# Optimization experiments

Hardware: AMD Instinct MI355X
Metric: run time of the kernel (lower is better)

## Reference

```python
import jax, jax.numpy as jnp
import numpy as np

WIN = 7          # window_size
DIM = 192        # embedding dim
HEADS = 6
HEAD_DIM = DIM // HEADS
B_ = 4096        # batch * num_windows
N = WIN * WIN    # tokens per window


def _relative_position_index():
    coords = np.stack(np.meshgrid(np.arange(WIN), np.arange(WIN), indexing='ij'))  # [2,7,7]
    flat = coords.reshape(2, -1)                                                   # [2,49]
    rel = flat[:, :, None] - flat[:, None, :]                                      # [2,49,49]
    rel = rel.transpose(1, 2, 0).astype(np.int32)                                  # [49,49,2]
    rel[:, :, 0] += WIN - 1
    rel[:, :, 1] += WIN - 1
    rel[:, :, 0] *= 2 * WIN - 1
    return jnp.asarray(rel.sum(-1), dtype=jnp.int32)                               # [49,49]


def setup_inputs() -> dict:
    key = jax.random.key(0)
    ks = jax.random.split(key, 6)
    std = 0.02
    return {
        'x': jax.random.normal(ks[0], (B_, N, DIM), dtype=jnp.float32),
        'qkv_w': jax.random.normal(ks[1], (3 * DIM, DIM), dtype=jnp.float32) * std,
        'qkv_b': jnp.zeros((3 * DIM,), dtype=jnp.float32),
        'proj_w': jax.random.normal(ks[2], (DIM, DIM), dtype=jnp.float32) * std,
        'proj_b': jnp.zeros((DIM,), dtype=jnp.float32),
        'bias_table': jax.random.normal(ks[3], ((2 * WIN - 1) ** 2, HEADS), dtype=jnp.float32) * std,
        'rel_index': _relative_position_index(),
    }


def reference(x, qkv_w, qkv_b, proj_w, proj_b, bias_table, rel_index):
    B, n, C = x.shape
    # qkv projection -> [3, B, H, N, hd]
    qkv = (x @ qkv_w.T + qkv_b).reshape(B, n, 3, HEADS, HEAD_DIM)
    qkv = jnp.transpose(qkv, (2, 0, 3, 1, 4))
    q, k, v = qkv[0], qkv[1], qkv[2]
    # relative position bias: [H, N, N]
    bias = bias_table[rel_index.reshape(-1)].reshape(n, n, HEADS)
    bias = jnp.transpose(bias, (2, 0, 1))[None]  # [1, H, N, N]
    scale = 1.0 / jnp.sqrt(jnp.asarray(HEAD_DIM, dtype=x.dtype))
    logits = jnp.einsum('bhnd,bhmd->bhnm', q, k) * scale + bias
    attn = jax.nn.softmax(logits, axis=-1)
    out = jnp.einsum('bhnm,bhmd->bhnd', attn, v)
    out = jnp.transpose(out, (0, 2, 1, 3)).reshape(B, n, C)
    return out @ proj_w.T + proj_b
```

## Files before the change

### kernel.cpp

```cpp
#include <hip/hip_runtime.h>

#define NTOK 49
#define DIM 192
#define HEADS 6
#define HD 32

typedef __bf16 bf16x8 __attribute__((ext_vector_type(8)));
typedef float f32x4 __attribute__((ext_vector_type(4)));

#define WPROJ_USH 110592
#define BIAS_BYTE 294912

#define SCALE 0.17677669529663687f

__device__ __forceinline__ unsigned short f2bf(float f) {
    unsigned int u = __builtin_bit_cast(unsigned int, f);
    u += 0x7fffu + ((u >> 16) & 1u);
    return (unsigned short)(u >> 16);
}
__device__ __forceinline__ unsigned int pack2(float a, float b) {
    return (unsigned int)f2bf(a) | ((unsigned int)f2bf(b) << 16);
}

__global__ void prep(const float* __restrict__ qkv_w, const float* __restrict__ proj_w,
                     const float* __restrict__ bias_table, const int* __restrict__ rel_index,
                     unsigned short* __restrict__ w16, float* __restrict__ bias_cd) {
    int bid = blockIdx.x;
    if (bid < 72) {
        int c = bid * 256 + threadIdx.x;
        const float* src; unsigned short* dst; int OT; int cc; int isq = 0;
        if (c < 13824)      { src = qkv_w;  dst = w16;             OT = 36; cc = c; isq = 1; }
        else                { src = proj_w; dst = w16 + WPROJ_USH; OT = 12; cc = c - 13824; }
        int lane = cc & 63;
        int t = cc >> 6;
        int ot = t % OT, ks = t / OT;
        int f  = ot * 16 + (lane & 15);
        int k0 = ks * 32 + (lane >> 4) * 8;
        float sc = (isq && f < 192) ? SCALE : 1.0f;
        const float* p = src + (size_t)f * DIM + k0;
        float4 a = *(const float4*)p;
        float4 b = *(const float4*)(p + 4);
        uint4 o;
        o.x = pack2(a.x * sc, a.y * sc); o.y = pack2(a.z * sc, a.w * sc);
        o.z = pack2(b.x * sc, b.y * sc); o.w = pack2(b.z * sc, b.w * sc);
        *(uint4*)(dst + (size_t)cc * 8) = o;
    } else {
        int gid = (bid - 72) * 256 + threadIdx.x;
        int lane = gid & 63;
        int tile = (gid >> 6) & 15;
        int h    = gid >> 10;
        int kt = tile >> 2, qt = tile & 3;
        int qtok = qt * 16 + (lane & 15);
        int key0 = kt * 16 + (lane >> 4) * 4;
        float4 v;
        float* vp = (float*)&v;
        for (int r = 0; r < 4; ++r) {
            int key = key0 + r;
            float val;
            if (key >= NTOK)       val = -1e30f;
            else if (qtok >= NTOK) val = 0.0f;
            else                   val = bias_table[rel_index[qtok * NTOK + key] * HEADS + h];
            vp[r] = val;
        }
        *(float4*)(bias_cd + (size_t)gid * 4) = v;
    }
}

#define SCR_OFF 24576
#define LDS_BYTES 49152

__global__ __launch_bounds__(384, 3) void win_attn(
    const float* __restrict__ x,
    const float* __restrict__ qkv_b,
    const float* __restrict__ proj_b,
    const unsigned short* __restrict__ wq16,
    const unsigned short* __restrict__ wp16,
    const float* __restrict__ bias_cd,
    float* __restrict__ out)
{
    extern __shared__ char smem[];
    const int tid  = threadIdx.x;
    const int lane = tid & 63;
    const int h    = tid >> 6;
    const int l15  = lane & 15;
    const int quad = lane >> 4;
    const int b    = blockIdx.x;

    for (int i = 0; i < 4; ++i) {
        int c  = tid + i * 384;
        int cl = c & 63;
        int mt = (c >> 6) & 3;
        int ks = c >> 8;
        int tok = mt * 16 + (cl & 15);
        int d0  = ks * 32 + (cl >> 4) * 8;
        uint4 o = {0u, 0u, 0u, 0u};
        if (tok < NTOK) {
            const float* p = x + ((size_t)b * NTOK + tok) * DIM + d0;
            float4 a  = *(const float4*)p;
            float4 bb = *(const float4*)(p + 4);
            o.x = pack2(a.x, a.y); o.y = pack2(a.z, a.w);
            o.z = pack2(bb.x, bb.y); o.w = pack2(bb.z, bb.w);
        }
        *(uint4*)(smem + (size_t)c * 16) = o;
    }
    __syncthreads();

    char* buf = smem + SCR_OFF + h * 4096;

    f32x4 qa[2][4], ka[2][4];
    for (int ft = 0; ft < 2; ++ft)
        for (int nt = 0; nt < 4; ++nt) { qa[ft][nt] = (f32x4){0,0,0,0}; ka[ft][nt] = (f32x4){0,0,0,0}; }
    for (int ks = 0; ks < 6; ++ks) {
        int4 xf[4];
        for (int nt = 0; nt < 4; ++nt)
            xf[nt] = *(const int4*)(smem + (((ks*4 + nt)*64 + lane) << 4));
        int4 wq[2], wk[2];
        for (int ft = 0; ft < 2; ++ft) {
            wq[ft] = *(const int4*)(wq16 + ((size_t)((ks*36      + h*2 + ft)*64 + lane) << 3));
            wk[ft] = *(const int4*)(wq16 + ((size_t)((ks*36 + 12 + h*2 + ft)*64 + lane) << 3));
        }
        for (int ft = 0; ft < 2; ++ft)
            for (int nt = 0; nt < 4; ++nt) {
                qa[ft][nt] = __builtin_amdgcn_mfma_f32_16x16x32_bf16(
                    __builtin_bit_cast(bf16x8, wq[ft]), __builtin_bit_cast(bf16x8, xf[nt]), qa[ft][nt], 0, 0, 0);
                ka[ft][nt] = __builtin_amdgcn_mfma_f32_16x16x32_bf16(
                    __builtin_bit_cast(bf16x8, wk[ft]), __builtin_bit_cast(bf16x8, xf[nt]), ka[ft][nt], 0, 0, 0);
            }
    }

    int4 qf[4], kf[4];
    for (int ft = 0; ft < 2; ++ft) {
        float4 bias = *(const float4*)(qkv_b + (h*2 + ft)*16 + quad*4);
        int quadp = ft*2 + (quad >> 1);
        for (int nt = 0; nt < 4; ++nt) {
            uint2 w;
            w.x = pack2(qa[ft][nt][0] + bias.x*SCALE, qa[ft][nt][1] + bias.y*SCALE);
            w.y = pack2(qa[ft][nt][2] + bias.z*SCALE, qa[ft][nt][3] + bias.w*SCALE);
            *(uint2*)(buf + nt*1024 + (l15 + 16*quadp)*16 + (quad & 1)*8) = w;
        }
    }
    for (int qt = 0; qt < 4; ++qt)
        qf[qt] = *(const int4*)(buf + qt*1024 + lane*16);
    for (int ft = 0; ft < 2; ++ft) {
        float4 bias = *(const float4*)(qkv_b + 192 + (h*2 + ft)*16 + quad*4);
        int quadp = ft*2 + (quad >> 1);
        for (int nt = 0; nt < 4; ++nt) {
            uint2 w;
            w.x = pack2(ka[ft][nt][0] + bias.x, ka[ft][nt][1] + bias.y);
            w.y = pack2(ka[ft][nt][2] + bias.z, ka[ft][nt][3] + bias.w);
            *(uint2*)(buf + nt*1024 + (l15 + 16*quadp)*16 + (quad & 1)*8) = w;
        }
    }
    for (int kt = 0; kt < 4; ++kt)
        kf[kt] = *(const int4*)(buf + kt*1024 + lane*16);

    f32x4 s[4][4];
    for (int kt = 0; kt < 4; ++kt)
        for (int qt = 0; qt < 4; ++qt) {
            f32x4 z = {0, 0, 0, 0};
            s[kt][qt] = __builtin_amdgcn_mfma_f32_16x16x32_bf16(
                __builtin_bit_cast(bf16x8, kf[kt]), __builtin_bit_cast(bf16x8, qf[qt]), z, 0, 0, 0);
        }
    for (int kt = 0; kt < 4; ++kt)
        for (int qt = 0; qt < 4; ++qt) {
            float4 bc = *(const float4*)(bias_cd + ((size_t)((h*16 + kt*4 + qt)*64 + lane) << 2));
            s[kt][qt][0] += bc.x; s[kt][qt][1] += bc.y;
            s[kt][qt][2] += bc.z; s[kt][qt][3] += bc.w;
        }
    float inv[4];
    for (int qt = 0; qt < 4; ++qt) {
        float sum = 0.f;
        for (int kt = 0; kt < 4; ++kt)
            for (int r = 0; r < 4; ++r) {
                float e = __expf(s[kt][qt][r]);
                s[kt][qt][r] = e;
                sum += e;
            }
        sum += __shfl_xor(sum, 16);
        sum += __shfl_xor(sum, 32);
        inv[qt] = 1.0f / sum;
    }
    int4 pf[2][4];
    for (int ksn = 0; ksn < 2; ++ksn) {
        for (int kt2 = 0; kt2 < 2; ++kt2) {
            int kt = ksn*2 + kt2;
            int quadp = kt2*2 + (quad >> 1);
            for (int qt = 0; qt < 4; ++qt) {
                uint2 w;
                w.x = pack2(s[kt][qt][0], s[kt][qt][1]);
                w.y = pack2(s[kt][qt][2], s[kt][qt][3]);
                *(uint2*)(buf + qt*1024 + (l15 + 16*quadp)*16 + (quad & 1)*8) = w;
            }
        }
        for (int qt = 0; qt < 4; ++qt)
            pf[ksn][qt] = *(const int4*)(buf + qt*1024 + lane*16);
    }

    f32x4 va[4][2];
    for (int mt = 0; mt < 4; ++mt)
        for (int nv = 0; nv < 2; ++nv) va[mt][nv] = (f32x4){0,0,0,0};
    for (int ks = 0; ks < 6; ++ks) {
        int4 xf[4];
        for (int mt = 0; mt < 4; ++mt)
            xf[mt] = *(const int4*)(smem + (((ks*4 + mt)*64 + lane) << 4));
        int4 wv[2];
        for (int nv = 0; nv < 2; ++nv)
            wv[nv] = *(const int4*)(wq16 + ((size_t)((ks*36 + 24 + h*2 + nv)*64 + lane) << 3));
        for (int mt = 0; mt < 4; ++mt)
            for (int nv = 0; nv < 2; ++nv)
                va[mt][nv] = __builtin_amdgcn_mfma_f32_16x16x32_bf16(
                    __builtin_bit_cast(bf16x8, xf[mt]), __builtin_bit_cast(bf16x8, wv[nv]), va[mt][nv], 0, 0, 0);
    }
    for (int nv = 0; nv < 2; ++nv) {
        float bias = qkv_b[384 + h*32 + nv*16 + l15];
        for (int mt = 0; mt < 4; ++mt) {
            int ksn = mt >> 1;
            int quadp = (mt & 1)*2 + (quad >> 1);
            uint2 w;
            w.x = pack2(va[mt][nv][0] + bias, va[mt][nv][1] + bias);
            w.y = pack2(va[mt][nv][2] + bias, va[mt][nv][3] + bias);
            *(uint2*)(buf + (ksn*2 + nv)*1024 + (l15 + 16*quadp)*16 + (quad & 1)*8) = w;
        }
    }
    int4 vf[2][2];
    for (int ksn = 0; ksn < 2; ++ksn)
        for (int dmt = 0; dmt < 2; ++dmt)
            vf[ksn][dmt] = *(const int4*)(buf + (ksn*2 + dmt)*1024 + lane*16);

    f32x4 oacc[2][4];
    for (int dmt = 0; dmt < 2; ++dmt)
        for (int qt = 0; qt < 4; ++qt) oacc[dmt][qt] = (f32x4){0, 0, 0, 0};
    for (int ksn = 0; ksn < 2; ++ksn)
        for (int dmt = 0; dmt < 2; ++dmt)
            for (int qt = 0; qt < 4; ++qt)
                oacc[dmt][qt] = __builtin_amdgcn_mfma_f32_16x16x32_bf16(
                    __builtin_bit_cast(bf16x8, vf[ksn][dmt]),
                    __builtin_bit_cast(bf16x8, pf[ksn][qt]), oacc[dmt][qt], 0, 0, 0);
    __syncthreads();

    for (int dmt = 0; dmt < 2; ++dmt) {
        int quadp = dmt*2 + (quad >> 1);
        for (int qt = 0; qt < 4; ++qt) {
            uint2 w;
            w.x = pack2(oacc[dmt][qt][0] * inv[qt], oacc[dmt][qt][1] * inv[qt]);
            w.y = pack2(oacc[dmt][qt][2] * inv[qt], oacc[dmt][qt][3] * inv[qt]);
            *(uint2*)(smem + (h*4 + qt)*1024 + (l15 + 16*quadp)*16 + (quad & 1)*8) = w;
        }
    }
    __syncthreads();

    {
        int no2 = h * 2;
        f32x4 acc[4][2];
        for (int mt = 0; mt < 4; ++mt)
            for (int j = 0; j < 2; ++j) acc[mt][j] = (f32x4){0, 0, 0, 0};
        for (int ks = 0; ks < 6; ++ks) {
            int4 oa[4];
            for (int mt = 0; mt < 4; ++mt)
                oa[mt] = *(const int4*)(smem + (ks*4 + mt)*1024 + lane*16);
            for (int j = 0; j < 2; ++j) {
                int4 wb = *(const int4*)(wp16 + ((size_t)((ks*12 + no2 + j)*64 + lane) << 3));
                bf16x8 bfr = __builtin_bit_cast(bf16x8, wb);
                for (int mt = 0; mt < 4; ++mt)
                    acc[mt][j] = __builtin_amdgcn_mfma_f32_16x16x32_bf16(
                        __builtin_bit_cast(bf16x8, oa[mt]), bfr, acc[mt][j], 0, 0, 0);
            }
        }
        for (int j = 0; j < 2; ++j) {
            int o = (no2 + j) * 16 + l15;
            float pb = proj_b[o];
            for (int mt = 0; mt < 4; ++mt) {
                int t0 = mt * 16 + quad * 4;
                for (int r = 0; r < 4; ++r) {
                    int t = t0 + r;
                    if (t < NTOK)
                        out[((size_t)b * NTOK + t) * DIM + o] = acc[mt][j][r] + pb;
                }
            }
        }
    }
}

extern "C" void kernel_launch(void* const* d_in, const int* in_sizes, int n_in,
                              void* d_out, int out_size, void* d_ws, size_t ws_size,
                              hipStream_t stream) {
    const float* x          = (const float*)d_in[0];
    const float* qkv_w      = (const float*)d_in[1];
    const float* qkv_b      = (const float*)d_in[2];
    const float* proj_w     = (const float*)d_in[3];
    const float* proj_b     = (const float*)d_in[4];
    const float* bias_table = (const float*)d_in[5];
    const int*   rel_index  = (const int*)d_in[6];
    float* out = (float*)d_out;

    unsigned short* w16 = (unsigned short*)d_ws;
    float* bias_cd = (float*)((char*)d_ws + BIAS_BYTE);

    prep<<<96, 256, 0, stream>>>(qkv_w, proj_w, bias_table, rel_index, w16, bias_cd);

    (void)hipFuncSetAttribute((const void*)win_attn,
                              hipFuncAttributeMaxDynamicSharedMemorySize, LDS_BYTES);
    win_attn<<<4096, 384, LDS_BYTES, stream>>>(x, qkv_b, proj_b,
                                               w16, w16 + WPROJ_USH, bias_cd, out);
}
```

Before: 457.0 us.

## Shrink per-wave scratch LDS and restructure phases to raise occupancy

Per-head scratch drops from 4 KB to 1 KB. Q, K, P and V tiles are now transposed through LDS one tile at a time, so total LDS falls from 48 KB to 30 KB and launch bounds rise from 3 to 5 blocks per CU. Q and K projections are computed in separate scoped phases, and the score MFMA is fused with bias add, exp and bf16 packing, which shortens register live ranges. It also switches to the hardware bf16 conversion cast and adds full unrolling. The risk is register spilling under the tighter bound, and more serialized LDS write/read round-trips.

```diff
diff --git a/kernel.cpp b/kernel.cpp
--- a/kernel.cpp
+++ b/kernel.cpp
@@ -13,13 +13,15 @@
 
 #define SCALE 0.17677669529663687f
 
-__device__ __forceinline__ unsigned short f2bf(float f) {
-    unsigned int u = __builtin_bit_cast(unsigned int, f);
-    u += 0x7fffu + ((u >> 16) & 1u);
-    return (unsigned short)(u >> 16);
-}
 __device__ __forceinline__ unsigned int pack2(float a, float b) {
-    return (unsigned int)f2bf(a) | ((unsigned int)f2bf(b) << 16);
+    unsigned short lo = __builtin_bit_cast(unsigned short, (__bf16)a);
+    unsigned short hi = __builtin_bit_cast(unsigned short, (__bf16)b);
+    return (unsigned int)lo | ((unsigned int)hi << 16);
+}
+
+__device__ __forceinline__ f32x4 mfma16(int4 a, int4 b, f32x4 c) {
+    return __builtin_amdgcn_mfma_f32_16x16x32_bf16(
+        __builtin_bit_cast(bf16x8, a), __builtin_bit_cast(bf16x8, b), c, 0, 0, 0);
 }
 
 __global__ void prep(const float* __restrict__ qkv_w, const float* __restrict__ proj_w,
@@ -67,9 +69,9 @@
 }
 
 #define SCR_OFF 24576
-#define LDS_BYTES 49152
-
-__global__ __launch_bounds__(384, 3) void win_attn(
+#define LDS_BYTES 30720
+
+__global__ __launch_bounds__(384, 5) void win_attn(
     const float* __restrict__ x,
     const float* __restrict__ qkv_b,
     const float* __restrict__ proj_b,
@@ -86,6 +88,7 @@
     const int quad = lane >> 4;
     const int b    = blockIdx.x;
 
+    #pragma unroll
     for (int i = 0; i < 4; ++i) {
         int c  = tid + i * 384;
         int cl = c & 63;
@@ -105,174 +108,222 @@
     }
     __syncthreads();
 
-    char* buf = smem + SCR_OFF + h * 4096;
-
-    f32x4 qa[2][4], ka[2][4];
-    for (int ft = 0; ft < 2; ++ft)
-        for (int nt = 0; nt < 4; ++nt) { qa[ft][nt] = (f32x4){0,0,0,0}; ka[ft][nt] = (f32x4){0,0,0,0}; }
-    for (int ks = 0; ks < 6; ++ks) {
-        int4 xf[4];
-        for (int nt = 0; nt < 4; ++nt)
-            xf[nt] = *(const int4*)(smem + (((ks*4 + nt)*64 + lane) << 4));
-        int4 wq[2], wk[2];
+    char* const xrd = smem + lane * 16;
+    char* const buf = smem + SCR_OFF + h * 1024;
+    char* const swr = buf + (quad & 1) * 8 + l15 * 16 + (quad >> 1) * 256;
+    char* const srd = buf + lane * 16;
+    const unsigned short* const wqh = wq16 + (size_t)(h * 128 + lane) * 8;
+    const unsigned short* const wph = wp16 + (size_t)(h * 128 + lane) * 8;
+
+    int4 qf[4];
+    {
+        f32x4 qa[2][4];
+        #pragma unroll
+        for (int ft = 0; ft < 2; ++ft)
+            #pragma unroll
+            for (int nt = 0; nt < 4; ++nt) qa[ft][nt] = (f32x4){0,0,0,0};
+        #pragma unroll
+        for (int ks = 0; ks < 6; ++ks) {
+            int4 wq[2];
+            #pragma unroll
+            for (int ft = 0; ft < 2; ++ft)
+                wq[ft] = *(const int4*)(wqh + (ks*36 + ft) * 512);
+            #pragma unroll
+            for (int nt = 0; nt < 4; ++nt) {
+                int4 xf = *(const int4*)(xrd + (ks*4 + nt) * 1024);
+                #pragma unroll
+                for (int ft = 0; ft < 2; ++ft)
+                    qa[ft][nt] = mfma16(wq[ft], xf, qa[ft][nt]);
+            }
+        }
+        float4 bq[2];
+        #pragma unroll
         for (int ft = 0; ft < 2; ++ft) {
-            wq[ft] = *(const int4*)(wq16 + ((size_t)((ks*36      + h*2 + ft)*64 + lane) << 3));
-            wk[ft] = *(const int4*)(wq16 + ((size_t)((ks*36 + 12 + h*2 + ft)*64 + lane) << 3));
-        }
+            float4 t = *(const float4*)(qkv_b + (h*2 + ft)*16 + quad*4);
+            bq[ft].x = t.x*SCALE; bq[ft].y = t.y*SCALE; bq[ft].z = t.z*SCALE; bq[ft].w = t.w*SCALE;
+        }
+        #pragma unroll
+        for (int nt = 0; nt < 4; ++nt) {
+            #pragma unroll
+            for (int ft = 0; ft < 2; ++ft) {
+                uint2 w;
+                w.x = pack2(qa[ft][nt][0] + bq[ft].x, qa[ft][nt][1] + bq[ft].y);
+                w.y = pack2(qa[ft][nt][2] + bq[ft].z, qa[ft][nt][3] + bq[ft].w);
+                *(uint2*)(swr + ft * 512) = w;
+            }
+            qf[nt] = *(const int4*)srd;
+        }
+    }
+
+    int4 kf[4];
+    {
+        f32x4 ka[2][4];
+        #pragma unroll
         for (int ft = 0; ft < 2; ++ft)
+            #pragma unroll
+            for (int nt = 0; nt < 4; ++nt) ka[ft][nt] = (f32x4){0,0,0,0};
+        #pragma unroll
+        for (int ks = 0; ks < 6; ++ks) {
+            int4 wk[2];
+            #pragma unroll
+            for (int ft = 0; ft < 2; ++ft)
+                wk[ft] = *(const int4*)(wqh + (ks*36 + ft) * 512 + 6144);
+            #pragma unroll
             for (int nt = 0; nt < 4; ++nt) {
-                qa[ft][nt] = __builtin_amdgcn_mfma_f32_16x16x32_bf16(
-                    __builtin_bit_cast(bf16x8, wq[ft]), __builtin_bit_cast(bf16x8, xf[nt]), qa[ft][nt], 0, 0, 0);
-                ka[ft][nt] = __builtin_amdgcn_mfma_f32_16x16x32_bf16(
-                    __builtin_bit_cast(bf16x8, wk[ft]), __builtin_bit_cast(bf16x8, xf[nt]), ka[ft][nt], 0, 0, 0);
-            }
-    }
-
-    int4 qf[4], kf[4];
-    for (int ft = 0; ft < 2; ++ft) {
-        float4 bias = *(const float4*)(qkv_b + (h*2 + ft)*16 + quad*4);
-        int quadp = ft*2 + (quad >> 1);
+                int4 xf = *(const int4*)(xrd + (ks*4 + nt) * 1024);
+                #pragma unroll
+                for (int ft = 0; ft < 2; ++ft)
+                    ka[ft][nt] = mfma16(wk[ft], xf, ka[ft][nt]);
+            }
+        }
+        float4 bk[2];
+        #pragma unroll
+        for (int ft = 0; ft < 2; ++ft)
+            bk[ft] = *(const float4*)(qkv_b + 192 + (h*2 + ft)*16 + quad*4);
+        #pragma unroll
         for (int nt = 0; nt < 4; ++nt) {
-            uint2 w;
-            w.x = pack2(qa[ft][nt][0] + bias.x*SCALE, qa[ft][nt][1] + bias.y*SCALE);
-            w.y = pack2(qa[ft][nt][2] + bias.z*SCALE, qa[ft][nt][3] + bias.w*SCALE);
-            *(uint2*)(buf + nt*1024 + (l15 + 16*quadp)*16 + (quad & 1)*8) = w;
-        }
-    }
-    for (int qt = 0; qt < 4; ++qt)
-        qf[qt] = *(const int4*)(buf + qt*1024 + lane*16);
-    for (int ft = 0; ft < 2; ++ft) {
-        float4 bias = *(const float4*)(qkv_b + 192 + (h*2 + ft)*16 + quad*4);
-        int quadp = ft*2 + (quad >> 1);
-        for (int nt = 0; nt < 4; ++nt) {
-            uint2 w;
-            w.x = pack2(ka[ft][nt][0] + bias.x, ka[ft][nt][1] + bias.y);
-            w.y = pack2(ka[ft][nt][2] + bias.z, ka[ft][nt][3] + bias.w);
-            *(uint2*)(buf + nt*1024 + (l15 + 16*quadp)*16 + (quad & 1)*8) = w;
-        }
-    }
-    for (int kt = 0; kt < 4; ++kt)
-        kf[kt] = *(const int4*)(buf + kt*1024 + lane*16);
-
-    f32x4 s[4][4];
-    for (int kt = 0; kt < 4; ++kt)
-        for (int qt = 0; qt < 4; ++qt) {
-            f32x4 z = {0, 0, 0, 0};
-            s[kt][qt] = __builtin_amdgcn_mfma_f32_16x16x32_bf16(
-                __builtin_bit_cast(bf16x8, kf[kt]), __builtin_bit_cast(bf16x8, qf[qt]), z, 0, 0, 0);
-        }
-    for (int kt = 0; kt < 4; ++kt)
-        for (int qt = 0; qt < 4; ++qt) {
-            float4 bc = *(const float4*)(bias_cd + ((size_t)((h*16 + kt*4 + qt)*64 + lane) << 2));
-            s[kt][qt][0] += bc.x; s[kt][qt][1] += bc.y;
-            s[kt][qt][2] += bc.z; s[kt][qt][3] += bc.w;
-        }
+            #pragma unroll
+            for (int ft = 0; ft < 2; ++ft) {
+                uint2 w;
+                w.x = pack2(ka[ft][nt][0] + bk[ft].x, ka[ft][nt][1] + bk[ft].y);
+                w.y = pack2(ka[ft][nt][2] + bk[ft].z, ka[ft][nt][3] + bk[ft].w);
+                *(uint2*)(swr + ft * 512) = w;
+            }
+            kf[nt] = *(const int4*)srd;
+        }
+    }
+
     float inv[4];
+    int4 pf[2][4];
+    const float* const bcb = bias_cd + (size_t)(h * 1024 + lane) * 4;
+    #pragma unroll
     for (int qt = 0; qt < 4; ++qt) {
         float sum = 0.f;
-        for (int kt = 0; kt < 4; ++kt)
-            for (int r = 0; r < 4; ++r) {
-                float e = __expf(s[kt][qt][r]);
-                s[kt][qt][r] = e;
-                sum += e;
-            }
+        #pragma unroll
+        for (int ksn = 0; ksn < 2; ++ksn) {
+            #pragma unroll
+            for (int kt2 = 0; kt2 < 2; ++kt2) {
+                const int kt = ksn*2 + kt2;
+                f32x4 z = {0,0,0,0};
+                f32x4 s = mfma16(kf[kt], qf[qt], z);
+                float4 bc = *(const float4*)(bcb + (kt*4 + qt) * 256);
+                float e0 = __expf(s[0] + bc.x);
+                float e1 = __expf(s[1] + bc.y);
+                float e2 = __expf(s[2] + bc.z);
+                float e3 = __expf(s[3] + bc.w);
+                sum += (e0 + e1) + (e2 + e3);
+                uint2 w;
+                w.x = pack2(e0, e1);
+                w.y = pack2(e2, e3);
+                *(uint2*)(swr + kt2 * 512) = w;
+            }
+            pf[ksn][qt] = *(const int4*)srd;
+        }
         sum += __shfl_xor(sum, 16);
         sum += __shfl_xor(sum, 32);
         inv[qt] = 1.0f / sum;
     }
-    int4 pf[2][4];
-    for (int ksn = 0; ksn < 2; ++ksn) {
-        for (int kt2 = 0; kt2 < 2; ++kt2) {
-            int kt = ksn*2 + kt2;
-            int quadp = kt2*2 + (quad >> 1);
+
+    int4 vf[2][2];
+    {
+        f32x4 va[4][2];
+        #pragma unroll
+        for (int mt = 0; mt < 4; ++mt)
+            #pragma unroll
+            for (int nv = 0; nv < 2; ++nv) va[mt][nv] = (f32x4){0,0,0,0};
+        #pragma unroll
+        for (int ks = 0; ks < 6; ++ks) {
+            int4 wv[2];
+            #pragma unroll
+            for (int nv = 0; nv < 2; ++nv)
+                wv[nv] = *(const int4*)(wqh + (ks*36 + nv) * 512 + 12288);
+            #pragma unroll
+            for (int mt = 0; mt < 4; ++mt) {
+                int4 xf = *(const int4*)(xrd + (ks*4 + mt) * 1024);
+                #pragma unroll
+                for (int nv = 0; nv < 2; ++nv)
+                    va[mt][nv] = mfma16(xf, wv[nv], va[mt][nv]);
+            }
+        }
+        const float bv0 = qkv_b[384 + h*32 + l15];
+        const float bv1 = qkv_b[384 + h*32 + 16 + l15];
+        #pragma unroll
+        for (int ksn = 0; ksn < 2; ++ksn) {
+            #pragma unroll
+            for (int nv = 0; nv < 2; ++nv) {
+                const float bv = nv ? bv1 : bv0;
+                #pragma unroll
+                for (int mt2 = 0; mt2 < 2; ++mt2) {
+                    const int mt = ksn*2 + mt2;
+                    uint2 w;
+                    w.x = pack2(va[mt][nv][0] + bv, va[mt][nv][1] + bv);
+                    w.y = pack2(va[mt][nv][2] + bv, va[mt][nv][3] + bv);
+                    *(uint2*)(swr + mt2 * 512) = w;
+                }
+                vf[ksn][nv] = *(const int4*)srd;
+            }
+        }
+    }
+
+    f32x4 oacc[2][4];
+    #pragma unroll
+    for (int dmt = 0; dmt < 2; ++dmt)
+        #pragma unroll
+        for (int qt = 0; qt < 4; ++qt) oacc[dmt][qt] = (f32x4){0, 0, 0, 0};
+    #pragma unroll
+    for (int ksn = 0; ksn < 2; ++ksn)
+        #pragma unroll
+        for (int dmt = 0; dmt < 2; ++dmt)
+            #pragma unroll
+            for (int qt = 0; qt < 4; ++qt)
+                oacc[dmt][qt] = mfma16(vf[ksn][dmt], pf[ksn][qt], oacc[dmt][qt]);
+    __syncthreads();
+
+    {
+        char* const owr = smem + (quad & 1) * 8 + l15 * 16 + (quad >> 1) * 256;
+        #pragma unroll
+        for (int dmt = 0; dmt < 2; ++dmt) {
+            #pragma unroll
             for (int qt = 0; qt < 4; ++qt) {
                 uint2 w;
-                w.x = pack2(s[kt][qt][0], s[kt][qt][1]);
-                w.y = pack2(s[kt][qt][2], s[kt][qt][3]);
-                *(uint2*)(buf + qt*1024 + (l15 + 16*quadp)*16 + (quad & 1)*8) = w;
-            }
-        }
-        for (int qt = 0; qt < 4; ++qt)
-            pf[ksn][qt] = *(const int4*)(buf + qt*1024 + lane*16);
-    }
-
-    f32x4 va[4][2];
-    for (int mt = 0; mt < 4; ++mt)
-        for (int nv = 0; nv < 2; ++nv) va[mt][nv] = (f32x4){0,0,0,0};
-    for (int ks = 0; ks < 6; ++ks) {
-        int4 xf[4];
+                w.x = pack2(oacc[dmt][qt][0] * inv[qt], oacc[dmt][qt][1] * inv[qt]);
+                w.y = pack2(oacc[dmt][qt][2] * inv[qt], oacc[dmt][qt][3] * inv[qt]);
+                *(uint2*)(owr + (h*4 + qt) * 1024 + dmt * 512) = w;
+            }
+        }
+    }
+    __syncthreads();
+
+    {
+        f32x4 acc[4][2];
+        #pragma unroll
         for (int mt = 0; mt < 4; ++mt)
-            xf[mt] = *(const int4*)(smem + (((ks*4 + mt)*64 + lane) << 4));
-        int4 wv[2];
-        for (int nv = 0; nv < 2; ++nv)
-            wv[nv] = *(const int4*)(wq16 + ((size_t)((ks*36 + 24 + h*2 + nv)*64 + lane) << 3));
-        for (int mt = 0; mt < 4; ++mt)
-            for (int nv = 0; nv < 2; ++nv)
-                va[mt][nv] = __builtin_amdgcn_mfma_f32_16x16x32_bf16(
-                    __builtin_bit_cast(bf16x8, xf[mt]), __builtin_bit_cast(bf16x8, wv[nv]), va[mt][nv], 0, 0, 0);
-    }
-    for (int nv = 0; nv < 2; ++nv) {
-        float bias = qkv_b[384 + h*32 + nv*16 + l15];
-        for (int mt = 0; mt < 4; ++mt) {
-            int ksn = mt >> 1;
-            int quadp = (mt & 1)*2 + (quad >> 1);
-            uint2 w;
-            w.x = pack2(va[mt][nv][0] + bias, va[mt][nv][1] + bias);
-            w.y = pack2(va[mt][nv][2] + bias, va[mt][nv][3] + bias);
-            *(uint2*)(buf + (ksn*2 + nv)*1024 + (l15 + 16*quadp)*16 + (quad & 1)*8) = w;
-        }
-    }
-    int4 vf[2][2];
-    for (int ksn = 0; ksn < 2; ++ksn)
-        for (int dmt = 0; dmt < 2; ++dmt)
-            vf[ksn][dmt] = *(const int4*)(buf + (ksn*2 + dmt)*1024 + lane*16);
-
-    f32x4 oacc[2][4];
-    for (int dmt = 0; dmt < 2; ++dmt)
-        for (int qt = 0; qt < 4; ++qt) oacc[dmt][qt] = (f32x4){0, 0, 0, 0};
-    for (int ksn = 0; ksn < 2; ++ksn)
-        for (int dmt = 0; dmt < 2; ++dmt)
-            for (int qt = 0; qt < 4; ++qt)
-                oacc[dmt][qt] = __builtin_amdgcn_mfma_f32_16x16x32_bf16(
-                    __builtin_bit_cast(bf16x8, vf[ksn][dmt]),
-                    __builtin_bit_cast(bf16x8, pf[ksn][qt]), oacc[dmt][qt], 0, 0, 0);
-    __syncthreads();
-
-    for (int dmt = 0; dmt < 2; ++dmt) {
-        int quadp = dmt*2 + (quad >> 1);
-        for (int qt = 0; qt < 4; ++qt) {
-            uint2 w;
-            w.x = pack2(oacc[dmt][qt][0] * inv[qt], oacc[dmt][qt][1] * inv[qt]);
-            w.y = pack2(oacc[dmt][qt][2] * inv[qt], oacc[dmt][qt][3] * inv[qt]);
-            *(uint2*)(smem + (h*4 + qt)*1024 + (l15 + 16*quadp)*16 + (quad & 1)*8) = w;
-        }
-    }
-    __syncthreads();
-
-    {
-        int no2 = h * 2;
-        f32x4 acc[4][2];
-        for (int mt = 0; mt < 4; ++mt)
+            #pragma unroll
             for (int j = 0; j < 2; ++j) acc[mt][j] = (f32x4){0, 0, 0, 0};
+        #pragma unroll
         for (int ks = 0; ks < 6; ++ks) {
-            int4 oa[4];
-            for (int mt = 0; mt < 4; ++mt)
-                oa[mt] = *(const int4*)(smem + (ks*4 + mt)*1024 + lane*16);
-            for (int j = 0; j < 2; ++j) {
-                int4 wb = *(const int4*)(wp16 + ((size_t)((ks*12 + no2 + j)*64 + lane) << 3));
-                bf16x8 bfr = __builtin_bit_cast(bf16x8, wb);
-                for (int mt = 0; mt < 4; ++mt)
-                    acc[mt][j] = __builtin_amdgcn_mfma_f32_16x16x32_bf16(
-                        __builtin_bit_cast(bf16x8, oa[mt]), bfr, acc[mt][j], 0, 0, 0);
-            }
-        }
+            int4 wb[2];
+            #pragma unroll
+            for (int j = 0; j < 2; ++j)
+                wb[j] = *(const int4*)(wph + (ks*12 + j) * 512);
+            #pragma unroll
+            for (int mt = 0; mt < 4; ++mt) {
+                int4 oa = *(const int4*)(xrd + (ks*4 + mt) * 1024);
+                #pragma unroll
+                for (int j = 0; j < 2; ++j)
+                    acc[mt][j] = mfma16(oa, wb[j], acc[mt][j]);
+            }
+        }
+        #pragma unroll
         for (int j = 0; j < 2; ++j) {
-            int o = (no2 + j) * 16 + l15;
-            float pb = proj_b[o];
+            const int o = (h*2 + j) * 16 + l15;
+            const float pb = proj_b[o];
+            #pragma unroll
             for (int mt = 0; mt < 4; ++mt) {
-                int t0 = mt * 16 + quad * 4;
+                const int t0 = mt * 16 + quad * 4;
+                #pragma unroll
                 for (int r = 0; r < 4; ++r) {
-                    int t = t0 + r;
+                    const int t = t0 + r;
                     if (t < NTOK)
                         out[((size_t)b * NTOK + t) * DIM + o] = acc[mt][j][r] + pb;
                 }
```

Result: slower. 734.5 us (+60.7%).
